# Optimization experiments

Measured on AMD Instinct MI355X. Metric: run time of the kernel, lower is better.

Reference implementation:

```python
import jax, jax.numpy as jnp
import numpy as np

D_PAIR = 128
N_HEAD = 4
D_HID = 32
SCALING = 1.0 / np.sqrt(D_HID)


def setup_inputs() -> dict:
    key = jax.random.key(0)
    ks = jax.random.split(key, 12)
    B, L = 1, 256
    s = 0.02
    return {
        "pair": jax.random.normal(ks[0], (B, L, L, D_PAIR), dtype=jnp.float32),
        "gamma": jnp.ones((D_PAIR,), jnp.float32),
        "beta": jnp.zeros((D_PAIR,), jnp.float32),
        "Wq": jax.random.normal(ks[1], (D_PAIR, N_HEAD * D_HID), jnp.float32) * s,
        "Wk": jax.random.normal(ks[2], (D_PAIR, N_HEAD * D_HID), jnp.float32) * s,
        "Wv": jax.random.normal(ks[3], (D_PAIR, N_HEAD * D_HID), jnp.float32) * s,
        "Wb": jax.random.normal(ks[4], (D_PAIR, N_HEAD), jnp.float32) * s,
        "Wg": jax.random.normal(ks[5], (D_PAIR, N_HEAD * D_HID), jnp.float32) * s,
        "bg": jnp.ones((N_HEAD * D_HID,), jnp.float32),
        "Wo": jax.random.normal(ks[6], (N_HEAD * D_HID, D_PAIR), jnp.float32) * s,
        "bo": jnp.zeros((D_PAIR,), jnp.float32),
    }


def _layernorm(x, gamma, beta, eps=1e-5):
    mu = jnp.mean(x, axis=-1, keepdims=True)
    var = jnp.var(x, axis=-1, keepdims=True)
    return (x - mu) * jax.lax.rsqrt(var + eps) * gamma + beta


def reference(pair, gamma, beta, Wq, Wk, Wv, Wb, Wg, bg, Wo, bo):
    B, L = pair.shape[:2]
    x = _layernorm(pair, gamma, beta)                      # (B,L,L,D)
    q = (x @ Wq).reshape(B, L, L, N_HEAD, D_HID) * SCALING  # (B,L,L,h,d)
    k = (x @ Wk).reshape(B, L, L, N_HEAD, D_HID)
    v = (x @ Wv).reshape(B, L, L, N_HEAD, D_HID)
    bias = x @ Wb                                           # (B,L,L,h)
    gate = jax.nn.sigmoid(x @ Wg + bg)                      # (B,L,L,h*d)
    # start_node=True: attend over ending index k of row i
    attn = jnp.einsum('bijhd,bikhd->bijkh', q, k)           # (B,L,L,L,h)
    attn = attn + bias[:, None]                             # bias[b,j,k,h] broadcast over i
    attn = jax.nn.softmax(attn, axis=-2)                    # over k
    out = jnp.einsum('bijkh,bikhd->bijhd', attn, v).reshape(B, L, L, N_HEAD * D_HID)
    out = gate * out
    return out @ Wo + bo
```

## Files before the change

kernel.cpp:

```cpp
#include <hip/hip_runtime.h>
#include <math.h>

#define L 256
#define DP 128
#define NH 4
#define DH 32
#define NROW 65536

typedef unsigned short ushort_t;
typedef __attribute__((ext_vector_type(8))) short short8;
typedef __attribute__((ext_vector_type(4))) float f32x4;

constexpr float SCALING = 0.17677669529663687f;

static __device__ __forceinline__ unsigned short f2bf(float f) {
    unsigned u = __builtin_bit_cast(unsigned, f);
    u = u + 0x7fffu + ((u >> 16) & 1u);
    return (unsigned short)(u >> 16);
}
static __device__ __forceinline__ float bf2f(unsigned short h) {
    unsigned u = ((unsigned)h) << 16;
    return __builtin_bit_cast(float, u);
}

__global__ __launch_bounds__(256) void prep_kernel(
    const float* __restrict__ Wq, const float* __restrict__ Wk, const float* __restrict__ Wv,
    const float* __restrict__ Wb, const float* __restrict__ Wg, const float* __restrict__ Wo,
    ushort_t* __restrict__ WtAll, ushort_t* __restrict__ WohT, ushort_t* __restrict__ WolT)
{
    int rowi = blockIdx.x * 16 + (threadIdx.x >> 4);
    int d0 = (threadIdx.x & 15) * 8;
    #pragma unroll
    for (int dd = 0; dd < 8; ++dd) {
        int d = d0 + dd;
        if (rowi < 512) {
            int n = rowi & 127;
            float val;
            if (rowi < 128)      val = Wq[d * 128 + n] * SCALING;
            else if (rowi < 256) val = Wk[d * 128 + n];
            else if (rowi < 384) val = Wv[d * 128 + n];
            else                 val = Wg[d * 128 + n];
            WtAll[rowi * 128 + d] = f2bf(val);
        } else if (rowi < 516) {
            WtAll[rowi * 128 + d] = f2bf(Wb[d * 4 + (rowi - 512)]);
        } else if (rowi < 528) {
            WtAll[rowi * 128 + d] = 0;
        } else if (rowi < 656) {
            int n = rowi - 528;
            WohT[n * 128 + d] = f2bf(Wo[d * 128 + n]);
        } else {
            int n = rowi - 656;
            float wv = Wo[d * 128 + n];
            unsigned short hb = f2bf(wv);
            WolT[n * 128 + d] = f2bf(wv - bf2f(hb));
        }
    }
}

__global__ __launch_bounds__(256) void ln_proj_mfma(
    const float* __restrict__ pair, const float* __restrict__ gamma, const float* __restrict__ beta,
    const ushort_t* __restrict__ WtAll, const float* __restrict__ bgv,
    ushort_t* __restrict__ qo, ushort_t* __restrict__ ko, ushort_t* __restrict__ vo,
    float* __restrict__ gateo, float* __restrict__ biasT)
{
    __shared__ __align__(16) unsigned char xs[64 * 256];

    const int t = threadIdx.x;
    const int w = t >> 6, lane = t & 63;
    const int c = lane & 15, g = lane >> 4;
    const int base = blockIdx.x * 64;

    {
        const float* pr = pair + ((size_t)base + w * 16) * DP;
        float e0[16], e1[16];
        #pragma unroll
        for (int r = 0; r < 16; ++r) {
            e0[r] = pr[r * DP + lane];
            e1[r] = pr[r * DP + 64 + lane];
        }
        const float g0 = gamma[lane], g1 = gamma[lane + 64];
        const float b0 = beta[lane],  b1 = beta[lane + 64];
        #pragma unroll
        for (int r = 0; r < 16; ++r) {
            float s = e0[r] + e1[r], ss = e0[r] * e0[r] + e1[r] * e1[r];
            #pragma unroll
            for (int o = 32; o > 0; o >>= 1) { s += __shfl_xor(s, o); ss += __shfl_xor(ss, o); }
            float mu = s * (1.f / DP);
            float rq = rsqrtf(ss * (1.f / DP) - mu * mu + 1e-5f);
            int rl = w * 16 + r;
            unsigned swz = (unsigned)((rl & 7) << 4);
            *(ushort_t*)(xs + (((unsigned)(rl * 256 + 2 * lane)) ^ swz)) = f2bf((e0[r] - mu) * rq * g0 + b0);
            *(ushort_t*)(xs + (((unsigned)(rl * 256 + 2 * (lane + 64))) ^ swz)) = f2bf((e1[r] - mu) * rq * g1 + b1);
        }
    }
    __syncthreads();

    short8 af[4];
    {
        int rl = w * 16 + c;
        unsigned swz = (unsigned)((rl & 7) << 4);
        #pragma unroll
        for (int kk = 0; kk < 4; ++kk)
            af[kk] = *(const short8*)(xs + (((unsigned)(rl * 256 + kk * 64 + g * 16)) ^ swz));
    }

    const int rowb = base + w * 16 + 4 * g;
    for (int nt = 0; nt < 33; ++nt) {
        f32x4 acc = {0.f, 0.f, 0.f, 0.f};
        const ushort_t* wb = WtAll + (size_t)(nt * 16 + c) * 128 + 8 * g;
        #pragma unroll
        for (int kk = 0; kk < 4; ++kk)
            acc = __builtin_amdgcn_mfma_f32_16x16x32_bf16(af[kk], *(const short8*)(wb + kk * 32), acc, 0, 0, 0);

        int n = nt * 16 + c;
        if (nt < 8) {
            #pragma unroll
            for (int e = 0; e < 4; ++e) qo[(size_t)(rowb + e) * 128 + n] = f2bf(acc[e]);
        } else if (nt < 16) {
            #pragma unroll
            for (int e = 0; e < 4; ++e) ko[(size_t)(rowb + e) * 128 + (n - 128)] = f2bf(acc[e]);
        } else if (nt < 24) {
            #pragma unroll
            for (int e = 0; e < 4; ++e) vo[(size_t)(rowb + e) * 128 + (n - 256)] = f2bf(acc[e]);
        } else if (nt < 32) {
            float bgn = bgv[n - 384];
            #pragma unroll
            for (int e = 0; e < 4; ++e)
                gateo[(size_t)(rowb + e) * 128 + (n - 384)] = 1.f / (1.f + __expf(-(acc[e] + bgn)));
        } else {
            if (c < 4) {
                #pragma unroll
                for (int e = 0; e < 4; ++e) biasT[(size_t)c * NROW + rowb + e] = acc[e];
            }
        }
    }
}

__global__ __launch_bounds__(256) void attn_mfma(
    const ushort_t* __restrict__ qbf, const ushort_t* __restrict__ kbf, const ushort_t* __restrict__ vbf,
    const float* __restrict__ biasT, float* __restrict__ ao)
{
    __shared__ __align__(16) unsigned char Kb[256 * 64];
    __shared__ __align__(16) unsigned char Vt[32 * 512];
    __shared__ __align__(16) unsigned char Plds[4 * 64 * 80];

    const int h = blockIdx.x & 3, i = blockIdx.x >> 2;
    const int t = threadIdx.x, w = t >> 6, lane = t & 63;
    const int c = lane & 15, g = lane >> 4;

    {
        const ushort_t* kg = kbf + (size_t)(i * 256) * 128 + h * 32;
        #pragma unroll
        for (int it = 0; it < 8; ++it) {
            int idx = it * 256 + t;
            int kr = idx >> 3, dp = idx & 7;
            *(uint2*)(Kb + kr * 64 + dp * 8) = *(const uint2*)(kg + (size_t)kr * 128 + dp * 4);
        }
    }
    {
        const ushort_t* vg = vbf + (size_t)(i * 256) * 128 + h * 32;
        #pragma unroll
        for (int it = 0; it < 4; ++it) {
            int idx = it * 256 + t;
            int kp = idx >> 3, dp = idx & 7;
            int kt = kp >> 4, cc = kp & 15;
            int r0 = kt * 32 + cc;
            uint2 a = *(const uint2*)(vg + (size_t)r0 * 128 + dp * 4);
            uint2 b = *(const uint2*)(vg + (size_t)(r0 + 16) * 128 + dp * 4);
            unsigned av[4] = { a.x & 0xffffu, a.x >> 16, a.y & 0xffffu, a.y >> 16 };
            unsigned bv[4] = { b.x & 0xffffu, b.x >> 16, b.y & 0xffffu, b.y >> 16 };
            int kcolb = kt * 64 + 4 * cc;
            #pragma unroll
            for (int dd = 0; dd < 4; ++dd) {
                int d = 4 * dp + dd;
                unsigned pk = (bv[dd] << 16) | av[dd];
                *(unsigned*)(Vt + (((unsigned)(d * 512 + kcolb)) ^ ((unsigned)((d & 7) << 4)))) = pk;
            }
        }
    }
    __syncthreads();

    const int j0 = w * 64;
    short8 qf[4];
    {
        const ushort_t* qg = qbf + (size_t)(i * 256 + j0) * 128 + h * 32;
        #pragma unroll
        for (int jt = 0; jt < 4; ++jt)
            qf[jt] = *(const short8*)(qg + (size_t)(jt * 16 + c) * 128 + 8 * g);
    }

    unsigned char* Pw = Plds + w * 5120;
    const float* biasTh = biasT + (size_t)h * NROW;

    f32x4 O[4][2];
    f32x4 rsum[4];
    #pragma unroll
    for (int jt = 0; jt < 4; ++jt) {
        rsum[jt] = (f32x4){0.f, 0.f, 0.f, 0.f};
        O[jt][0] = (f32x4){0.f, 0.f, 0.f, 0.f};
        O[jt][1] = (f32x4){0.f, 0.f, 0.f, 0.f};
    }

    for (int kt = 0; kt < 8; ++kt) {
        short8 kf[2];
        #pragma unroll
        for (int ks = 0; ks < 2; ++ks)
            kf[ks] = *(const short8*)(Kb + (kt * 32 + ks * 16 + c) * 64 + g * 16);

        f32x4 s[4][2];
        #pragma unroll
        for (int jt = 0; jt < 4; ++jt) {
            #pragma unroll
            for (int ks = 0; ks < 2; ++ks) {
                f32x4 z = {0.f, 0.f, 0.f, 0.f};
                s[jt][ks] = __builtin_amdgcn_mfma_f32_16x16x32_bf16(qf[jt], kf[ks], z, 0, 0, 0);
            }
        }
        #pragma unroll
        for (int jt = 0; jt < 4; ++jt) {
            #pragma unroll
            for (int ks = 0; ks < 2; ++ks) {
                const float* bp = biasTh + (size_t)(j0 + jt * 16 + 4 * g) * 256 + kt * 32 + ks * 16 + c;
                #pragma unroll
                for (int e = 0; e < 4; ++e)
                    s[jt][ks][e] = __expf(s[jt][ks][e] + bp[e * 256]);
            }
            #pragma unroll
            for (int e = 0; e < 4; ++e) {
                rsum[jt][e] += s[jt][0][e] + s[jt][1][e];
                unsigned pk = ((unsigned)f2bf(s[jt][1][e]) << 16) | (unsigned)f2bf(s[jt][0][e]);
                *(unsigned*)(Pw + (jt * 16 + 4 * g + e) * 80 + 4 * c) = pk;
            }
        }
        short8 vb0, vb1;
        {
            int d_0 = c, d_1 = 16 + c;
            vb0 = *(const short8*)(Vt + (((unsigned)(d_0 * 512 + kt * 64 + g * 16)) ^ ((unsigned)((d_0 & 7) << 4))));
            vb1 = *(const short8*)(Vt + (((unsigned)(d_1 * 512 + kt * 64 + g * 16)) ^ ((unsigned)((d_1 & 7) << 4))));
        }
        #pragma unroll
        for (int jt = 0; jt < 4; ++jt) {
            short8 pa = *(const short8*)(Pw + (jt * 16 + c) * 80 + g * 16);
            O[jt][0] = __builtin_amdgcn_mfma_f32_16x16x32_bf16(pa, vb0, O[jt][0], 0, 0, 0);
            O[jt][1] = __builtin_amdgcn_mfma_f32_16x16x32_bf16(pa, vb1, O[jt][1], 0, 0, 0);
        }
    }

    #pragma unroll
    for (int jt = 0; jt < 4; ++jt) {
        #pragma unroll
        for (int e = 0; e < 4; ++e) {
            float v = rsum[jt][e];
            v += __shfl_xor(v, 1); v += __shfl_xor(v, 2);
            v += __shfl_xor(v, 4); v += __shfl_xor(v, 8);
            rsum[jt][e] = 1.f / v;
        }
    }
    float* aoB = ao + (size_t)(i * 256 + j0) * 128 + h * 32;
    #pragma unroll
    for (int jt = 0; jt < 4; ++jt) {
        #pragma unroll
        for (int dt = 0; dt < 2; ++dt) {
            #pragma unroll
            for (int e = 0; e < 4; ++e)
                aoB[(size_t)(jt * 16 + 4 * g + e) * 128 + dt * 16 + c] = O[jt][dt][e] * rsum[jt][e];
        }
    }
}

__global__ __launch_bounds__(256) void out_proj_mfma(
    const float* __restrict__ gate, const float* __restrict__ ao,
    const ushort_t* __restrict__ WohT, const ushort_t* __restrict__ WolT,
    const float* __restrict__ bo, float* __restrict__ out)
{
    __shared__ __align__(16) unsigned char xh[64 * 256];
    __shared__ __align__(16) unsigned char xl[64 * 256];

    const int t = threadIdx.x;
    const int w = t >> 6, lane = t & 63;
    const int c = lane & 15, g = lane >> 4;
    const int base = blockIdx.x * 64;

    #pragma unroll
    for (int it = 0; it < 8; ++it) {
        int idx = it * 256 + t;
        int row = idx >> 5, c4 = idx & 31;
        float4 gg = *(const float4*)(gate + (size_t)(base + row) * 128 + c4 * 4);
        float4 aa = *(const float4*)(ao + (size_t)(base + row) * 128 + c4 * 4);
        float x0 = gg.x * aa.x, x1 = gg.y * aa.y, x2 = gg.z * aa.z, x3 = gg.w * aa.w;
        unsigned short h0 = f2bf(x0), h1 = f2bf(x1), h2 = f2bf(x2), h3 = f2bf(x3);
        unsigned short l0 = f2bf(x0 - bf2f(h0)), l1 = f2bf(x1 - bf2f(h1));
        unsigned short l2 = f2bf(x2 - bf2f(h2)), l3 = f2bf(x3 - bf2f(h3));
        unsigned swz = (unsigned)((row & 7) << 4);
        uint2 hv = { ((unsigned)h1 << 16) | h0, ((unsigned)h3 << 16) | h2 };
        uint2 lv = { ((unsigned)l1 << 16) | l0, ((unsigned)l3 << 16) | l2 };
        *(uint2*)(xh + (((unsigned)(row * 256 + c4 * 8)) ^ swz)) = hv;
        *(uint2*)(xl + (((unsigned)(row * 256 + c4 * 8)) ^ swz)) = lv;
    }
    __syncthreads();

    short8 ah[4], al[4];
    {
        int rl = w * 16 + c;
        unsigned swz = (unsigned)((rl & 7) << 4);
        #pragma unroll
        for (int kk = 0; kk < 4; ++kk) {
            ah[kk] = *(const short8*)(xh + (((unsigned)(rl * 256 + kk * 64 + g * 16)) ^ swz));
            al[kk] = *(const short8*)(xl + (((unsigned)(rl * 256 + kk * 64 + g * 16)) ^ swz));
        }
    }

    const int rowb = base + w * 16 + 4 * g;
    #pragma unroll 1
    for (int nt = 0; nt < 8; ++nt) {
        f32x4 acc = {0.f, 0.f, 0.f, 0.f};
        const ushort_t* wh = WohT + (size_t)(nt * 16 + c) * 128 + 8 * g;
        const ushort_t* wl = WolT + (size_t)(nt * 16 + c) * 128 + 8 * g;
        #pragma unroll
        for (int kk = 0; kk < 4; ++kk) {
            short8 bh = *(const short8*)(wh + kk * 32);
            short8 bl = *(const short8*)(wl + kk * 32);
            acc = __builtin_amdgcn_mfma_f32_16x16x32_bf16(ah[kk], bh, acc, 0, 0, 0);
            acc = __builtin_amdgcn_mfma_f32_16x16x32_bf16(ah[kk], bl, acc, 0, 0, 0);
            acc = __builtin_amdgcn_mfma_f32_16x16x32_bf16(al[kk], bh, acc, 0, 0, 0);
        }
        int n = nt * 16 + c;
        float bon = bo[n];
        #pragma unroll
        for (int e = 0; e < 4; ++e)
            out[(size_t)(rowb + e) * 128 + n] = acc[e] + bon;
    }
}

extern "C" void kernel_launch(void* const* d_in, const int* in_sizes, int n_in,
                              void* d_out, int out_size, void* d_ws, size_t ws_size,
                              hipStream_t stream) {
    const float* pair  = (const float*)d_in[0];
    const float* gamma = (const float*)d_in[1];
    const float* beta  = (const float*)d_in[2];
    const float* Wq    = (const float*)d_in[3];
    const float* Wk    = (const float*)d_in[4];
    const float* Wv    = (const float*)d_in[5];
    const float* Wb    = (const float*)d_in[6];
    const float* Wg    = (const float*)d_in[7];
    const float* bg    = (const float*)d_in[8];
    const float* Wo    = (const float*)d_in[9];
    const float* bo    = (const float*)d_in[10];

    unsigned char* ws = (unsigned char*)d_ws;
    size_t off = 0;
    ushort_t* q_bf   = (ushort_t*)(ws + off); off += (size_t)NROW * 128 * 2;
    ushort_t* k_bf   = (ushort_t*)(ws + off); off += (size_t)NROW * 128 * 2;
    ushort_t* v_bf   = (ushort_t*)(ws + off); off += (size_t)NROW * 128 * 2;
    float*    gateo  = (float*)(ws + off);    off += (size_t)NROW * 128 * 4;
    float*    ao     = (float*)(ws + off);    off += (size_t)NROW * 128 * 4;
    float*    biasT  = (float*)(ws + off);    off += (size_t)NH * NROW * 4;
    ushort_t* WtAll  = (ushort_t*)(ws + off); off += 528 * 128 * 2;
    ushort_t* WohT   = (ushort_t*)(ws + off); off += 128 * 128 * 2;
    ushort_t* WolT   = (ushort_t*)(ws + off); off += 128 * 128 * 2;

    prep_kernel<<<49, 256, 0, stream>>>(Wq, Wk, Wv, Wb, Wg, Wo, WtAll, WohT, WolT);
    ln_proj_mfma<<<NROW / 64, 256, 0, stream>>>(pair, gamma, beta, WtAll, bg,
                                                q_bf, k_bf, v_bf, gateo, biasT);
    attn_mfma<<<L * NH, 256, 0, stream>>>(q_bf, k_bf, v_bf, biasT, ao);
    out_proj_mfma<<<NROW / 64, 256, 0, stream>>>(gateo, ao, WohT, WolT, bo, (float*)d_out);
}
```

Before: 256.7 us.

## Reuse weight fragments across row groups, transpose bias layout, drop LDS staging in out-proj

The projection kernel now has each wave own a set of output column tiles and load their weight fragments once, reusing them across all four 16-row groups while reading activation fragments from LDS. The bias tensor is stored transposed so the attention kernel can fetch four bias values with one vector load instead of four strided scalar loads. The output projection builds its bf16 hi/lo A fragments straight from global memory, skipping the LDS round trip and barrier, and unrolls the N loop by two. These changes cut global weight traffic and load instruction count, at the cost of more LDS reads in the projection and less coalesced global reads in the out-proj.

```diff
diff --git a/kernel.cpp b/kernel.cpp
--- a/kernel.cpp
+++ b/kernel.cpp
@@ -95,42 +95,48 @@
     }
     __syncthreads();
 
-    short8 af[4];
-    {
-        int rl = w * 16 + c;
-        unsigned swz = (unsigned)((rl & 7) << 4);
-        #pragma unroll
-        for (int kk = 0; kk < 4; ++kk)
-            af[kk] = *(const short8*)(xs + (((unsigned)(rl * 256 + kk * 64 + g * 16)) ^ swz));
-    }
-
-    const int rowb = base + w * 16 + 4 * g;
-    for (int nt = 0; nt < 33; ++nt) {
-        f32x4 acc = {0.f, 0.f, 0.f, 0.f};
-        const ushort_t* wb = WtAll + (size_t)(nt * 16 + c) * 128 + 8 * g;
-        #pragma unroll
-        for (int kk = 0; kk < 4; ++kk)
-            acc = __builtin_amdgcn_mfma_f32_16x16x32_bf16(af[kk], *(const short8*)(wb + kk * 32), acc, 0, 0, 0);
-
-        int n = nt * 16 + c;
-        if (nt < 8) {
-            #pragma unroll
-            for (int e = 0; e < 4; ++e) qo[(size_t)(rowb + e) * 128 + n] = f2bf(acc[e]);
-        } else if (nt < 16) {
-            #pragma unroll
-            for (int e = 0; e < 4; ++e) ko[(size_t)(rowb + e) * 128 + (n - 128)] = f2bf(acc[e]);
-        } else if (nt < 24) {
-            #pragma unroll
-            for (int e = 0; e < 4; ++e) vo[(size_t)(rowb + e) * 128 + (n - 256)] = f2bf(acc[e]);
-        } else if (nt < 32) {
-            float bgn = bgv[n - 384];
-            #pragma unroll
-            for (int e = 0; e < 4; ++e)
-                gateo[(size_t)(rowb + e) * 128 + (n - 384)] = 1.f / (1.f + __expf(-(acc[e] + bgn)));
-        } else {
-            if (c < 4) {
-                #pragma unroll
-                for (int e = 0; e < 4; ++e) biasT[(size_t)c * NROW + rowb + e] = acc[e];
+    const int mtot = (w == 3) ? 9 : 8;
+    for (int m = 0; m < mtot; ++m) {
+        const int nt = (m < 8) ? (w + 4 * m) : 32;
+        const ushort_t* wbp = WtAll + (size_t)(nt * 16 + c) * 128 + 8 * g;
+        short8 bw[4];
+        #pragma unroll
+        for (int kk = 0; kk < 4; ++kk) bw[kk] = *(const short8*)(wbp + kk * 32);
+
+        const int n = nt * 16 + c;
+        #pragma unroll
+        for (int rg = 0; rg < 4; ++rg) {
+            const int rl = rg * 16 + c;
+            const unsigned swz = (unsigned)((rl & 7) << 4);
+            f32x4 acc = {0.f, 0.f, 0.f, 0.f};
+            #pragma unroll
+            for (int kk = 0; kk < 4; ++kk) {
+                short8 af = *(const short8*)(xs + (((unsigned)(rl * 256 + kk * 64 + g * 16)) ^ swz));
+                acc = __builtin_amdgcn_mfma_f32_16x16x32_bf16(af, bw[kk], acc, 0, 0, 0);
+            }
+            const int rowb = base + rg * 16 + 4 * g;
+            if (nt < 8) {
+                #pragma unroll
+                for (int e = 0; e < 4; ++e) qo[(size_t)(rowb + e) * 128 + n] = f2bf(acc[e]);
+            } else if (nt < 16) {
+                #pragma unroll
+                for (int e = 0; e < 4; ++e) ko[(size_t)(rowb + e) * 128 + (n - 128)] = f2bf(acc[e]);
+            } else if (nt < 24) {
+                #pragma unroll
+                for (int e = 0; e < 4; ++e) vo[(size_t)(rowb + e) * 128 + (n - 256)] = f2bf(acc[e]);
+            } else if (nt < 32) {
+                float bgn = bgv[n - 384];
+                #pragma unroll
+                for (int e = 0; e < 4; ++e)
+                    gateo[(size_t)(rowb + e) * 128 + (n - 384)] = 1.f / (1.f + __expf(-(acc[e] + bgn)));
+            } else {
+                if (c < 4) {
+                    #pragma unroll
+                    for (int e = 0; e < 4; ++e) {
+                        int r = rowb + e;
+                        biasT[(size_t)c * NROW + (r & 255) * 256 + (r >> 8)] = acc[e];
+                    }
+                }
             }
         }
     }
@@ -220,10 +226,10 @@
         for (int jt = 0; jt < 4; ++jt) {
             #pragma unroll
             for (int ks = 0; ks < 2; ++ks) {
-                const float* bp = biasTh + (size_t)(j0 + jt * 16 + 4 * g) * 256 + kt * 32 + ks * 16 + c;
+                const f32x4 bv = *(const f32x4*)(biasTh + (size_t)(kt * 32 + ks * 16 + c) * 256 + (j0 + jt * 16 + 4 * g));
                 #pragma unroll
                 for (int e = 0; e < 4; ++e)
-                    s[jt][ks][e] = __expf(s[jt][ks][e] + bp[e * 256]);
+                    s[jt][ks][e] = __expf(s[jt][ks][e] + bv[e]);
             }
             #pragma unroll
             for (int e = 0; e < 4; ++e) {
@@ -273,45 +279,33 @@
     const ushort_t* __restrict__ WohT, const ushort_t* __restrict__ WolT,
     const float* __restrict__ bo, float* __restrict__ out)
 {
-    __shared__ __align__(16) unsigned char xh[64 * 256];
-    __shared__ __align__(16) unsigned char xl[64 * 256];
-
     const int t = threadIdx.x;
     const int w = t >> 6, lane = t & 63;
     const int c = lane & 15, g = lane >> 4;
     const int base = blockIdx.x * 64;
 
-    #pragma unroll
-    for (int it = 0; it < 8; ++it) {
-        int idx = it * 256 + t;
-        int row = idx >> 5, c4 = idx & 31;
-        float4 gg = *(const float4*)(gate + (size_t)(base + row) * 128 + c4 * 4);
-        float4 aa = *(const float4*)(ao + (size_t)(base + row) * 128 + c4 * 4);
-        float x0 = gg.x * aa.x, x1 = gg.y * aa.y, x2 = gg.z * aa.z, x3 = gg.w * aa.w;
-        unsigned short h0 = f2bf(x0), h1 = f2bf(x1), h2 = f2bf(x2), h3 = f2bf(x3);
-        unsigned short l0 = f2bf(x0 - bf2f(h0)), l1 = f2bf(x1 - bf2f(h1));
-        unsigned short l2 = f2bf(x2 - bf2f(h2)), l3 = f2bf(x3 - bf2f(h3));
-        unsigned swz = (unsigned)((row & 7) << 4);
-        uint2 hv = { ((unsigned)h1 << 16) | h0, ((unsigned)h3 << 16) | h2 };
-        uint2 lv = { ((unsigned)l1 << 16) | l0, ((unsigned)l3 << 16) | l2 };
-        *(uint2*)(xh + (((unsigned)(row * 256 + c4 * 8)) ^ swz)) = hv;
-        *(uint2*)(xl + (((unsigned)(row * 256 + c4 * 8)) ^ swz)) = lv;
-    }
-    __syncthreads();
-
+    const size_t arow = (size_t)(base + w * 16 + c) * 128;
     short8 ah[4], al[4];
-    {
-        int rl = w * 16 + c;
-        unsigned swz = (unsigned)((rl & 7) << 4);
-        #pragma unroll
-        for (int kk = 0; kk < 4; ++kk) {
-            ah[kk] = *(const short8*)(xh + (((unsigned)(rl * 256 + kk * 64 + g * 16)) ^ swz));
-            al[kk] = *(const short8*)(xl + (((unsigned)(rl * 256 + kk * 64 + g * 16)) ^ swz));
-        }
+    #pragma unroll
+    for (int kk = 0; kk < 4; ++kk) {
+        const float* gp = gate + arow + kk * 32 + g * 8;
+        const float* ap = ao + arow + kk * 32 + g * 8;
+        f32x4 g0 = *(const f32x4*)gp, g1 = *(const f32x4*)(gp + 4);
+        f32x4 a0 = *(const f32x4*)ap, a1 = *(const f32x4*)(ap + 4);
+        short8 hv, lv;
+        #pragma unroll
+        for (int e = 0; e < 4; ++e) {
+            float x0 = g0[e] * a0[e];
+            float x1 = g1[e] * a1[e];
+            unsigned short h0 = f2bf(x0), h1 = f2bf(x1);
+            hv[e] = (short)h0; hv[e + 4] = (short)h1;
+            lv[e] = (short)f2bf(x0 - bf2f(h0)); lv[e + 4] = (short)f2bf(x1 - bf2f(h1));
+        }
+        ah[kk] = hv; al[kk] = lv;
     }
 
     const int rowb = base + w * 16 + 4 * g;
-    #pragma unroll 1
+    #pragma unroll 2
     for (int nt = 0; nt < 8; ++nt) {
         f32x4 acc = {0.f, 0.f, 0.f, 0.f};
         const ushort_t* wh = WohT + (size_t)(nt * 16 + c) * 128 + 8 * g;
```

Result: faster. 239.5 us (-6.7%).
